# Performance work log

Measured on AMD Instinct MI355X. Metric: run time of the kernel, lower is better.

Reference implementation:

```python
import jax, jax.numpy as jnp
from jax import lax
import numpy as np

N3, N2, N1, N0 = 862, 1723, 3445, 6890  # mesh hierarchy (SMPL 6890 verts)
DEG, K = 16, 4  # nnz/row per Chebyshev support; K = order 3 + 1 supports


def _conv(x, w, b, s):
    y = lax.conv_general_dilated(x, w, (s, s), 'VALID', dimension_numbers=('NCHW', 'OIHW', 'NCHW'))
    return y + b[None, :, None, None]


def _pool(x):
    return lax.reduce_window(x, -jnp.inf, lax.max, (1, 1, 2, 2), (1, 1, 2, 2), 'VALID')


def _lin(x, w, b):
    return x @ w.T + b


def _rodrigues(r):  # [J,3] axis-angle -> [J,3,3] (batch_rodrigues)
    th = jnp.linalg.norm(r, axis=1, keepdims=True) + 1e-8
    k = r / th
    kx, ky, kz = k[:, 0], k[:, 1], k[:, 2]
    z = jnp.zeros_like(kx)
    Km = jnp.stack([z, -kz, ky, kz, z, -kx, -ky, kx, z], axis=1).reshape(-1, 3, 3)
    th = th[:, :, None]
    return jnp.eye(3, dtype=r.dtype)[None] + jnp.sin(th) * Km + (1.0 - jnp.cos(th)) * (Km @ Km)


def _spmm(idx, val, x):  # torch.sparse.mm with fixed nnz/row; idx,val: [N,D]
    return jnp.einsum('nd,ndf->nf', val, x[idx])


def _gcl(x, idx, val, W, b):  # Chebyshev graph conv: sum_k (A_k @ x) @ W_k + b
    return jnp.einsum('knd,kndf,kfo->no', val, x[idx], W) + b


def _basenet(frame, p):
    (c1w, c1b, c2w, c2b, c3w, c3b, c4w, c4b, c5w, c5b, fc1w, fc1b, fc4w, fc4b) = p
    c = _pool(jax.nn.relu(_conv(frame, c1w, c1b, 2)))
    c = _pool(jax.nn.relu(_conv(c, c2w, c2b, 1)))
    c = _pool(jax.nn.relu(_conv(c, c3w, c3b, 1)))
    c = _pool(jax.nn.relu(_conv(c, c4w, c4b, 1)))
    c = _pool(_conv(c, c5w, c5b, 1))  # [1,128,14,14]
    flat = jnp.transpose(c, (0, 3, 2, 1)).reshape(1, -1)  # torch.transpose(c,1,-1).reshape(1,-1)
    return _lin(flat, fc1w, fc1b), jax.nn.relu(_lin(flat, fc4w, fc4b))


def _forward(segmentations, poses, pose_mean, trans,
             c1w, c1b, c2w, c2b, c3w, c3b, c4w, c4b, c5w, c5b,
             fc1w, fc1b, fc2w, fc2b, fc3w, fc3b, fc4w, fc4b,
             fc5w, fc5b, fc6w, fc6b, fc7w, fc7b,
             gW3, gb3, gW2, gb2, gW1, gb1, gW0, gb0,
             av3, av2, av1, av0, uv2, uv1, uv0,
             ai3, ai2, ai1, ai0, ui2, ui1, ui0):
    nf = segmentations.shape[0]
    bp = (c1w, c1b, c2w, c2b, c3w, c3b, c4w, c4b, c5w, c5b, fc1w, fc1b, fc4w, fc4b)
    shape20, pose200 = jax.vmap(lambda f: _basenet(f, bp))(segmentations)  # [F,1,20],[F,1,200]
    pose_feat = jax.nn.relu(_lin(poses, fc5w, fc5b))  # [F,1,200]
    cat = jnp.concatenate([pose200, pose_feat], axis=-1)  # [F,1,400]
    pose_results = _lin(_lin(cat, fc6w, fc6b), fc7w, fc7b)  # [F,1,219]
    pm = pose_mean.at[:3].set(0.0)
    pose_init = _rodrigues(pm.reshape(-1, 3)).reshape(-1)  # [216]
    pct = jnp.concatenate([trans, pose_init])[None, None]  # [1,1,219]
    add = pose_results + pct
    add_poses = add[..., 3:].reshape(nf, -1, 24, 3, 3)
    add_trans = add[..., :3]
    betas_avr = shape20.reshape(-1, 20).mean(0)  # [20]
    betas_val = _lin(betas_avr, fc3w, fc3b)[None]  # [1,10]
    x = _lin(betas_avr, fc2w, fc2b).reshape(N3, 64)
    x = jax.nn.relu(_gcl(x, ai3, av3, gW3, gb3))  # [862,32]
    x = _spmm(ui2, uv2, x)                         # [1723,32]
    x = jax.nn.relu(_gcl(x, ai2, av2, gW2, gb2))  # [1723,16]
    x = _spmm(ui1, uv1, x)                         # [3445,16]
    x = jax.nn.relu(_gcl(x, ai1, av1, gW1, gb1))  # [3445,16]
    x = _spmm(ui0, uv0, x)                         # [6890,16]
    x = jnp.tanh(_gcl(x, ai0, av0, gW0, gb0))     # [6890,3]
    offsets = (x / 10.0)[None]
    return offsets, betas_val, add_poses, add_trans


def setup_inputs():
    ks = iter(jax.random.split(jax.random.key(0), 80))
    f32 = jnp.float32
    nrm = lambda shp, s: jax.random.normal(next(ks), shp, f32) * s
    uni = lambda shp, s: jax.random.uniform(next(ks), shp, f32) * s
    ri = lambda shp, hi: jax.random.randint(next(ks), shp, 0, hi)
    inp = {}
    inp['segmentations'] = nrm((8, 1, 3, 1017, 1017), 1.0)
    inp['poses'] = nrm((8, 1, 75), 1.0)
    inp['pose_mean'] = nrm((72,), 0.3)
    inp['trans'] = jnp.array([0.0, 0.2, -2.3], f32)
    for nm, shp, s in [('c1w', (8, 3, 3, 3), .1), ('c1b', (8,), .01), ('c2w', (16, 8, 3, 3), .1), ('c2b', (16,), .01),
                       ('c3w', (32, 16, 3, 3), .1), ('c3b', (32,), .01), ('c4w', (64, 32, 3, 3), .1), ('c4b', (64,), .01),
                       ('c5w', (128, 64, 3, 3), .1), ('c5b', (128,), .01),
                       ('fc1w', (20, 25088), .01), ('fc1b', (20,), .01), ('fc2w', (55168, 20), .05), ('fc2b', (55168,), .01),
                       ('fc3w', (10, 20), .05), ('fc3b', (10,), .01), ('fc4w', (200, 25088), .01), ('fc4b', (200,), .01),
                       ('fc5w', (200, 75), .05), ('fc5b', (200,), .01), ('fc6w', (100, 400), .05), ('fc6b', (100,), .01),
                       ('fc7w', (219, 100), .05), ('fc7b', (219,), .01),
                       ('gW3', (4, 64, 32), .1), ('gb3', (32,), .01), ('gW2', (4, 32, 16), .1), ('gb2', (16,), .01),
                       ('gW1', (4, 16, 16), .1), ('gb1', (16,), .01), ('gW0', (4, 16, 3), .1), ('gb0', (3,), .01)]:
        inp[nm] = nrm(shp, s)
    for nm, n in [('3', N3), ('2', N2), ('1', N1), ('0', N0)]:
        inp['av' + nm] = uni((K, n, DEG), 0.2)
        inp['ai' + nm] = ri((K, n, DEG), n)
    for nm, n_fine, n_coarse in [('2', N2, N3), ('1', N1, N2), ('0', N0, N1)]:
        inp['uv' + nm] = uni((n_fine, 4), 0.3)
        inp['ui' + nm] = ri((n_fine, 4), n_coarse)
    return inp


def reference(segmentations, poses, pose_mean, trans,
              c1w, c1b, c2w, c2b, c3w, c3b, c4w, c4b, c5w, c5b,
              fc1w, fc1b, fc2w, fc2b, fc3w, fc3b, fc4w, fc4b,
              fc5w, fc5b, fc6w, fc6b, fc7w, fc7b,
              gW3, gb3, gW2, gb2, gW1, gb1, gW0, gb0,
              av3, av2, av1, av0, uv2, uv1, uv0,
              ai3, ai2, ai1, ai0, ui2, ui1, ui0):
    return _forward(segmentations, poses, pose_mean, trans,
                    c1w, c1b, c2w, c2b, c3w, c3b, c4w, c4b, c5w, c5b,
                    fc1w, fc1b, fc2w, fc2b, fc3w, fc3b, fc4w, fc4b,
                    fc5w, fc5b, fc6w, fc6b, fc7w, fc7b,
                    gW3, gb3, gW2, gb2, gW1, gb1, gW0, gb0,
                    av3, av2, av1, av0, uv2, uv1, uv0,
                    ai3, ai2, ai1, ai0, ui2, ui1, ui0)
```

## Files before the change

### kernel.cpp

```cpp
#include <hip/hip_runtime.h>
#include <math.h>

__global__ __launch_bounds__(256) void conv1_lds(
    const float* __restrict__ in, const float* __restrict__ w,
    const float* __restrict__ bias, float* __restrict__ out)
{
    constexpr int Hin = 1017, P = 254;
    __shared__ float li[17][4][65];
    const int f  = blockIdx.y;
    const int ct = blockIdx.x & 3;
    const int rt = blockIdx.x >> 2;
    const int t  = threadIdx.x;
    const int lane = t & 63, wid = t >> 6;
    const int row0 = rt * 16, col0 = ct * 256;
    const float* inf = in + (size_t)f * 3 * Hin * Hin;

    const int ph = rt * 4 + wid, pw = ct * 64 + lane;
    const bool wactive = (ph < P) && (pw < P);

    float acc[32];
    #pragma unroll
    for (int i = 0; i < 32; i++) acc[i] = 0.f;

    for (int ic = 0; ic < 3; ic++) {
        __syncthreads();
        const float* src = inf + (size_t)ic * Hin * Hin;
        #pragma unroll
        for (int i = 0; i < 17; i++) {
            int gr = row0 + i; if (gr > Hin - 1) gr = Hin - 1;
            int gc = col0 + t; if (gc > Hin - 1) gc = Hin - 1;
            li[i][t & 3][t >> 2] = src[(size_t)gr * Hin + gc];
        }
        if (t < 17) {
            int gr = row0 + t; if (gr > Hin - 1) gr = Hin - 1;
            int gc = col0 + 256; if (gc > Hin - 1) gc = Hin - 1;
            li[t][0][64] = src[(size_t)gr * Hin + gc];
        }
        __syncthreads();

        float win[25];
        #pragma unroll
        for (int r = 0; r < 5; r++)
            #pragma unroll
            for (int c = 0; c < 5; c++)
                win[r * 5 + c] = li[4 * wid + r][c & 3][lane + (c >> 2)];

        #pragma unroll
        for (int oc = 0; oc < 8; oc++) {
            float wr[9];
            #pragma unroll
            for (int j = 0; j < 9; j++) wr[j] = w[(oc * 3 + ic) * 9 + j];
            #pragma unroll
            for (int py = 0; py < 2; py++)
                #pragma unroll
                for (int px = 0; px < 2; px++) {
                    float s = acc[(oc * 2 + py) * 2 + px];
                    #pragma unroll
                    for (int kh = 0; kh < 3; kh++)
                        #pragma unroll
                        for (int kw = 0; kw < 3; kw++)
                            s += wr[kh * 3 + kw] * win[(2 * py + kh) * 5 + (2 * px + kw)];
                    acc[(oc * 2 + py) * 2 + px] = s;
                }
        }
    }

    if (wactive) {
        #pragma unroll
        for (int oc = 0; oc < 8; oc++) {
            float m = fmaxf(fmaxf(acc[oc * 4 + 0], acc[oc * 4 + 1]),
                            fmaxf(acc[oc * 4 + 2], acc[oc * 4 + 3]));
            m = fmaxf(m + bias[oc], 0.f);
            out[(((size_t)f * 8 + oc) * P + ph) * P + pw] = m;
        }
    }
}

template<int IC, int OCG, bool RELU, bool FLATOUT>
__global__ __launch_bounds__(256) void conv_pool_s1(
    const float* __restrict__ in, const float* __restrict__ w,
    const float* __restrict__ bias, float* __restrict__ out,
    int Hin, int P, int OC)
{
    const int f = blockIdx.y, g = blockIdx.z;
    int tid = blockIdx.x * 256 + threadIdx.x;
    if (tid >= P * P) return;
    int ph = tid / P, pw = tid % P;
    const float* inf = in + ((size_t)f * IC) * Hin * Hin + (size_t)(2 * ph) * Hin + 2 * pw;
    const float* wg = w + (size_t)g * OCG * IC * 9;

    float acc[OCG * 4];
    #pragma unroll
    for (int i = 0; i < OCG * 4; i++) acc[i] = 0.f;

    for (int ic = 0; ic < IC; ic++) {
        const float* p = inf + (size_t)ic * Hin * Hin;
        float win[4][4];
        #pragma unroll
        for (int r = 0; r < 4; r++) {
            float2 a = *(const float2*)(p + (size_t)r * Hin);
            float2 b = *(const float2*)(p + (size_t)r * Hin + 2);
            win[r][0] = a.x; win[r][1] = a.y; win[r][2] = b.x; win[r][3] = b.y;
        }
        #pragma unroll
        for (int oc = 0; oc < OCG; oc++) {
            float wr[9];
            #pragma unroll
            for (int j = 0; j < 9; j++) wr[j] = wg[(oc * IC + ic) * 9 + j];
            #pragma unroll
            for (int py = 0; py < 2; py++)
                #pragma unroll
                for (int px = 0; px < 2; px++) {
                    float s = acc[(oc * 2 + py) * 2 + px];
                    #pragma unroll
                    for (int kh = 0; kh < 3; kh++)
                        #pragma unroll
                        for (int kw = 0; kw < 3; kw++)
                            s += wr[kh * 3 + kw] * win[py + kh][px + kw];
                    acc[(oc * 2 + py) * 2 + px] = s;
                }
        }
    }

    #pragma unroll
    for (int oc = 0; oc < OCG; oc++) {
        float m = fmaxf(fmaxf(acc[oc * 4 + 0], acc[oc * 4 + 1]),
                        fmaxf(acc[oc * 4 + 2], acc[oc * 4 + 3]));
        m += bias[g * OCG + oc];
        if (RELU) m = fmaxf(m, 0.f);
        int ocg = g * OCG + oc;
        if (FLATOUT) {
            out[(size_t)f * (P * P * OC) + (pw * P + ph) * OC + ocg] = m;
        } else {
            out[(((size_t)f * OC + ocg) * P + ph) * P + pw] = m;
        }
    }
}

__global__ __launch_bounds__(256) void fc_head(
    const float* __restrict__ flat,
    const float* __restrict__ fc1w, const float* __restrict__ fc1b,
    const float* __restrict__ fc4w, const float* __restrict__ fc4b,
    float* __restrict__ shape20, float* __restrict__ pose200)
{
    int o = blockIdx.x;
    const float* W = (o < 20) ? fc1w + (size_t)o * 25088
                              : fc4w + (size_t)(o - 20) * 25088;
    const float4* W4  = (const float4*)W;
    const float4* fl4 = (const float4*)flat;
    float acc[8];
    #pragma unroll
    for (int f = 0; f < 8; f++) acc[f] = 0.f;
    for (int i = threadIdx.x; i < 6272; i += 256) {
        float4 wv = W4[i];
        #pragma unroll
        for (int f = 0; f < 8; f++) {
            float4 xv = fl4[f * 6272 + i];
            acc[f] += wv.x * xv.x + wv.y * xv.y + wv.z * xv.z + wv.w * xv.w;
        }
    }
    #pragma unroll
    for (int f = 0; f < 8; f++)
        for (int off = 32; off > 0; off >>= 1)
            acc[f] += __shfl_down(acc[f], off, 64);
    __shared__ float red[4][8];
    int wid = threadIdx.x >> 6, lane = threadIdx.x & 63;
    if (lane == 0) {
        #pragma unroll
        for (int f = 0; f < 8; f++) red[wid][f] = acc[f];
    }
    __syncthreads();
    if (threadIdx.x < 8) {
        int f = threadIdx.x;
        float s = red[0][f] + red[1][f] + red[2][f] + red[3][f];
        if (o < 20) shape20[f * 20 + o] = s + fc1b[o];
        else        pose200[f * 200 + (o - 20)] = fmaxf(s + fc4b[o - 20], 0.f);
    }
}

__global__ __launch_bounds__(256) void pose_fc5(
    const float* __restrict__ poses,
    const float* __restrict__ fc5w, const float* __restrict__ fc5b,
    float* __restrict__ pose_feat)
{
    int t = blockIdx.x * 256 + threadIdx.x;
    if (t >= 8 * 200) return;
    int f = t / 200, o = t % 200;
    float s = fc5b[o];
    const float* pr = poses + f * 75;
    const float* wr = fc5w + o * 75;
    #pragma unroll 5
    for (int j = 0; j < 75; j++) s += pr[j] * wr[j];
    pose_feat[f * 200 + o] = fmaxf(s, 0.f);
}

__global__ __launch_bounds__(256) void pose_fc6(
    const float* __restrict__ pose200, const float* __restrict__ pose_feat,
    const float* __restrict__ fc6w, const float* __restrict__ fc6b,
    float* __restrict__ t1)
{
    int wv = blockIdx.x * 4 + (threadIdx.x >> 6);
    int lane = threadIdx.x & 63;
    if (wv >= 8 * 100) return;
    int f = wv / 100, o = wv % 100;
    float s = 0.f;
    for (int j = lane; j < 400; j += 64) {
        float xv = (j < 200) ? pose200[f * 200 + j] : pose_feat[f * 200 + (j - 200)];
        s += xv * fc6w[o * 400 + j];
    }
    #pragma unroll
    for (int off = 32; off > 0; off >>= 1) s += __shfl_down(s, off, 64);
    if (lane == 0) t1[f * 100 + o] = s + fc6b[o];
}

__global__ __launch_bounds__(256) void pose_fc7(
    const float* __restrict__ t1, const float* __restrict__ fc7w,
    const float* __restrict__ fc7b, const float* __restrict__ pose_mean,
    const float* __restrict__ trans, float* __restrict__ out)
{
    int wv = blockIdx.x * 4 + (threadIdx.x >> 6);
    int lane = threadIdx.x & 63;
    if (wv >= 8 * 219) return;
    int f = wv / 219, c = wv % 219;
    float s = 0.f;
    {
        float xv = t1[f * 100 + lane];
        s += xv * fc7w[c * 100 + lane];
        int j2 = lane + 64;
        if (j2 < 100) s += t1[f * 100 + j2] * fc7w[c * 100 + j2];
    }
    #pragma unroll
    for (int off = 32; off > 0; off >>= 1) s += __shfl_down(s, off, 64);
    if (lane != 0) return;
    s += fc7b[c];
    float pct;
    if (c < 3) {
        pct = trans[c];
    } else {
        int j = (c - 3) / 9, e = (c - 3) % 9;
        float rx = (j == 0) ? 0.f : pose_mean[3 * j + 0];
        float ry = (j == 0) ? 0.f : pose_mean[3 * j + 1];
        float rz = (j == 0) ? 0.f : pose_mean[3 * j + 2];
        float th = sqrtf(rx * rx + ry * ry + rz * rz) + 1e-8f;
        float kx = rx / th, ky = ry / th, kz = rz / th;
        float sn = sinf(th), c2 = 1.f - cosf(th);
        float R[9];
        R[0] = 1.f - c2 * (ky * ky + kz * kz);
        R[1] = -sn * kz + c2 * (kx * ky);
        R[2] =  sn * ky + c2 * (kx * kz);
        R[3] =  sn * kz + c2 * (kx * ky);
        R[4] = 1.f - c2 * (kx * kx + kz * kz);
        R[5] = -sn * kx + c2 * (ky * kz);
        R[6] = -sn * ky + c2 * (kx * kz);
        R[7] =  sn * kx + c2 * (ky * kz);
        R[8] = 1.f - c2 * (kx * kx + ky * ky);
        pct = R[e];
    }
    s += pct;
    if (c < 3) out[22408 + f * 3 + c] = s;
    else       out[20680 + f * 216 + (c - 3)] = s;
}

__global__ __launch_bounds__(256) void betas_fc2(
    const float* __restrict__ shape20,
    const float* __restrict__ fc2w, const float* __restrict__ fc2b,
    const float* __restrict__ fc3w, const float* __restrict__ fc3b,
    float* __restrict__ x0, float* __restrict__ out)
{
    __shared__ float avr[20];
    int t = threadIdx.x;
    if (t < 20) {
        float s = 0.f;
        for (int f = 0; f < 8; f++) s += shape20[f * 20 + t];
        avr[t] = s * 0.125f;
    }
    __syncthreads();
    int r = blockIdx.x * 256 + t;
    if (r < 55168) {
        float s = fc2b[r];
        #pragma unroll
        for (int j = 0; j < 20; j++) s += fc2w[(size_t)r * 20 + j] * avr[j];
        x0[r] = s;
    }
    if (blockIdx.x == 0 && t < 10) {
        float s = fc3b[t];
        for (int j = 0; j < 20; j++) s += fc3w[t * 20 + j] * avr[j];
        out[20670 + t] = s;
    }
}

template<int F, int O, int ACT>
__global__ __launch_bounds__(256) void gcl(
    const float* __restrict__ x, const int* __restrict__ ai,
    const float* __restrict__ av, const float* __restrict__ gW,
    const float* __restrict__ gb, float* __restrict__ y, int N)
{
    constexpr int VPW = 64 / F;
    constexpr int VPB = 4 * VPW;
    constexpr int HS  = 4 * F + 8;
    __shared__ float h[VPB][HS];

    int wid = threadIdx.x >> 6, lane = threadIdx.x & 63;
    {
        int vl = wid * VPW + (VPW == 1 ? 0 : lane / F);
        int fl = lane % F;
        int n = blockIdx.x * VPB + vl;
        if (n < N) {
            #pragma unroll
            for (int k = 0; k < 4; k++) {
                const int*   ip = ai + ((size_t)k * N + n) * 16;
                const float* vp = av + ((size_t)k * N + n) * 16;
                float s = 0.f;
                #pragma unroll
                for (int d = 0; d < 16; d++)
                    s += vp[d] * x[(size_t)ip[d] * F + fl];
                h[vl][k * F + fl] = s;
            }
        }
    }
    __syncthreads();

    int t = threadIdx.x;
    if (t < VPB * O) {
        int vl = t / O, o = t % O;
        int n = blockIdx.x * VPB + vl;
        if (n < N) {
            float s = gb[o];
            #pragma unroll
            for (int k = 0; k < 4; k++)
                for (int f2 = 0; f2 < F; f2++)
                    s += h[vl][k * F + f2] * gW[((size_t)k * F + f2) * O + o];
            if (ACT == 0) s = fmaxf(s, 0.f);
            else          s = tanhf(s) * 0.1f;
            y[(size_t)n * O + o] = s;
        }
    }
}

template<int F>
__global__ __launch_bounds__(256) void spmm(
    const float* __restrict__ x, const int* __restrict__ ui,
    const float* __restrict__ uv, float* __restrict__ y, int N)
{
    int t = blockIdx.x * 256 + threadIdx.x;
    if (t >= N * F) return;
    int n = t / F, f = t % F;
    float s = 0.f;
    #pragma unroll
    for (int j = 0; j < 4; j++)
        s += uv[n * 4 + j] * x[(size_t)ui[n * 4 + j] * F + f];
    y[t] = s;
}

extern "C" void kernel_launch(void* const* d_in, const int* in_sizes, int n_in,
                              void* d_out, int out_size, void* d_ws, size_t ws_size,
                              hipStream_t stream) {
    (void)in_sizes; (void)n_in; (void)out_size; (void)ws_size;

    const float* seg   = (const float*)d_in[0];
    const float* poses = (const float*)d_in[1];
    const float* pmean = (const float*)d_in[2];
    const float* trans = (const float*)d_in[3];
    const float* c1w = (const float*)d_in[4];  const float* c1b = (const float*)d_in[5];
    const float* c2w = (const float*)d_in[6];  const float* c2b = (const float*)d_in[7];
    const float* c3w = (const float*)d_in[8];  const float* c3b = (const float*)d_in[9];
    const float* c4w = (const float*)d_in[10]; const float* c4b = (const float*)d_in[11];
    const float* c5w = (const float*)d_in[12]; const float* c5b = (const float*)d_in[13];
    const float* fc1w = (const float*)d_in[14]; const float* fc1b = (const float*)d_in[15];
    const float* fc2w = (const float*)d_in[16]; const float* fc2b = (const float*)d_in[17];
    const float* fc3w = (const float*)d_in[18]; const float* fc3b = (const float*)d_in[19];
    const float* fc4w = (const float*)d_in[20]; const float* fc4b = (const float*)d_in[21];
    const float* fc5w = (const float*)d_in[22]; const float* fc5b = (const float*)d_in[23];
    const float* fc6w = (const float*)d_in[24]; const float* fc6b = (const float*)d_in[25];
    const float* fc7w = (const float*)d_in[26]; const float* fc7b = (const float*)d_in[27];
    const float* gW3 = (const float*)d_in[28]; const float* gb3 = (const float*)d_in[29];
    const float* gW2 = (const float*)d_in[30]; const float* gb2 = (const float*)d_in[31];
    const float* gW1 = (const float*)d_in[32]; const float* gb1 = (const float*)d_in[33];
    const float* gW0 = (const float*)d_in[34]; const float* gb0 = (const float*)d_in[35];
    const float* av3 = (const float*)d_in[36]; const int* ai3 = (const int*)d_in[37];
    const float* av2 = (const float*)d_in[38]; const int* ai2 = (const int*)d_in[39];
    const float* av1 = (const float*)d_in[40]; const int* ai1 = (const int*)d_in[41];
    const float* av0 = (const float*)d_in[42]; const int* ai0 = (const int*)d_in[43];
    const float* uv2 = (const float*)d_in[44]; const int* ui2 = (const int*)d_in[45];
    const float* uv1 = (const float*)d_in[46]; const int* ui1 = (const int*)d_in[47];
    const float* uv0 = (const float*)d_in[48]; const int* ui0 = (const int*)d_in[49];

    float* W = (float*)d_ws;
    float* out = (float*)d_out;

    float* pool1 = W + 0;
    float* pool2 = W + 4129024;
    float* pool3 = W + 0;
    float* pool4 = W + 4129024;
    float* flat5 = W + 4589824;
    float* shape20 = W + 1000000;
    float* pose200 = shape20 + 160;
    float* x0  = pose200 + 1600;
    float* y3  = x0 + 55168;
    float* x2  = y3 + 27584;
    float* y2  = x2 + 55136;
    float* x1  = y2 + 27568;
    float* y1  = x1 + 55120;
    float* x0u = y1 + 55120;
    float* pose_feat = x0u + 110240;
    float* t1 = pose_feat + 1600;

    conv1_lds<<<dim3(256, 8), 256, 0, stream>>>(seg, c1w, c1b, pool1);
    conv_pool_s1<8, 16, true, false>
        <<<dim3(63, 8, 1), 256, 0, stream>>>(pool1, c2w, c2b, pool2, 254, 126, 16);
    conv_pool_s1<16, 16, true, false>
        <<<dim3(16, 8, 2), 256, 0, stream>>>(pool2, c3w, c3b, pool3, 126, 62, 32);
    conv_pool_s1<32, 8, true, false>
        <<<dim3(4, 8, 8), 256, 0, stream>>>(pool3, c4w, c4b, pool4, 62, 30, 64);
    conv_pool_s1<64, 2, false, true>
        <<<dim3(1, 8, 64), 256, 0, stream>>>(pool4, c5w, c5b, flat5, 30, 14, 128);

    fc_head<<<dim3(220), 256, 0, stream>>>(flat5, fc1w, fc1b, fc4w, fc4b, shape20, pose200);
    pose_fc5<<<dim3(7),   256, 0, stream>>>(poses, fc5w, fc5b, pose_feat);
    pose_fc6<<<dim3(200), 256, 0, stream>>>(pose200, pose_feat, fc6w, fc6b, t1);
    pose_fc7<<<dim3(438), 256, 0, stream>>>(t1, fc7w, fc7b, pmean, trans, out);
    betas_fc2<<<dim3(216), 256, 0, stream>>>(shape20, fc2w, fc2b, fc3w, fc3b, x0, out);

    gcl<64, 32, 0><<<dim3(216),  256, 0, stream>>>(x0,  ai3, av3, gW3, gb3, y3, 862);
    spmm<32>      <<<dim3(216),  256, 0, stream>>>(y3,  ui2, uv2, x2, 1723);
    gcl<32, 16, 0><<<dim3(216),  256, 0, stream>>>(x2,  ai2, av2, gW2, gb2, y2, 1723);
    spmm<16>      <<<dim3(216),  256, 0, stream>>>(y2,  ui1, uv1, x1, 3445);
    gcl<16, 16, 0><<<dim3(216),  256, 0, stream>>>(x1,  ai1, av1, gW1, gb1, y1, 3445);
    spmm<16>      <<<dim3(431),  256, 0, stream>>>(y1,  ui0, uv0, x0u, 6890);
    gcl<16, 3, 1> <<<dim3(431),  256, 0, stream>>>(x0u, ai0, av0, gW0, gb0, out, 6890);
}
```

Measured before the change: 192.6 us.

## Merge small FC kernels into combined launches and halve conv output-channel groups

```diff
diff --git a/kernel.cpp b/kernel.cpp
--- a/kernel.cpp
+++ b/kernel.cpp
@@ -137,80 +137,111 @@
     }
 }
 
-__global__ __launch_bounds__(256) void fc_head(
+__global__ __launch_bounds__(256) void fc_head_plus(
     const float* __restrict__ flat,
     const float* __restrict__ fc1w, const float* __restrict__ fc1b,
     const float* __restrict__ fc4w, const float* __restrict__ fc4b,
-    float* __restrict__ shape20, float* __restrict__ pose200)
-{
-    int o = blockIdx.x;
-    const float* W = (o < 20) ? fc1w + (size_t)o * 25088
-                              : fc4w + (size_t)(o - 20) * 25088;
-    const float4* W4  = (const float4*)W;
-    const float4* fl4 = (const float4*)flat;
-    float acc[8];
-    #pragma unroll
-    for (int f = 0; f < 8; f++) acc[f] = 0.f;
-    for (int i = threadIdx.x; i < 6272; i += 256) {
-        float4 wv = W4[i];
-        #pragma unroll
-        for (int f = 0; f < 8; f++) {
-            float4 xv = fl4[f * 6272 + i];
-            acc[f] += wv.x * xv.x + wv.y * xv.y + wv.z * xv.z + wv.w * xv.w;
-        }
-    }
-    #pragma unroll
-    for (int f = 0; f < 8; f++)
-        for (int off = 32; off > 0; off >>= 1)
-            acc[f] += __shfl_down(acc[f], off, 64);
-    __shared__ float red[4][8];
-    int wid = threadIdx.x >> 6, lane = threadIdx.x & 63;
-    if (lane == 0) {
-        #pragma unroll
-        for (int f = 0; f < 8; f++) red[wid][f] = acc[f];
-    }
-    __syncthreads();
-    if (threadIdx.x < 8) {
-        int f = threadIdx.x;
-        float s = red[0][f] + red[1][f] + red[2][f] + red[3][f];
-        if (o < 20) shape20[f * 20 + o] = s + fc1b[o];
-        else        pose200[f * 200 + (o - 20)] = fmaxf(s + fc4b[o - 20], 0.f);
-    }
-}
-
-__global__ __launch_bounds__(256) void pose_fc5(
     const float* __restrict__ poses,
     const float* __restrict__ fc5w, const float* __restrict__ fc5b,
+    float* __restrict__ shape20, float* __restrict__ pose200,
     float* __restrict__ pose_feat)
 {
-    int t = blockIdx.x * 256 + threadIdx.x;
-    if (t >= 8 * 200) return;
-    int f = t / 200, o = t % 200;
-    float s = fc5b[o];
-    const float* pr = poses + f * 75;
-    const float* wr = fc5w + o * 75;
-    #pragma unroll 5
-    for (int j = 0; j < 75; j++) s += pr[j] * wr[j];
-    pose_feat[f * 200 + o] = fmaxf(s, 0.f);
-}
-
-__global__ __launch_bounds__(256) void pose_fc6(
+    int o = blockIdx.x;
+    if (o < 220) {
+        const float* W = (o < 20) ? fc1w + (size_t)o * 25088
+                                  : fc4w + (size_t)(o - 20) * 25088;
+        const float4* W4  = (const float4*)W;
+        const float4* fl4 = (const float4*)flat;
+        float acc[8];
+        #pragma unroll
+        for (int f = 0; f < 8; f++) acc[f] = 0.f;
+        for (int i = threadIdx.x; i < 6272; i += 256) {
+            float4 wv = W4[i];
+            #pragma unroll
+            for (int f = 0; f < 8; f++) {
+                float4 xv = fl4[f * 6272 + i];
+                acc[f] += wv.x * xv.x + wv.y * xv.y + wv.z * xv.z + wv.w * xv.w;
+            }
+        }
+        #pragma unroll
+        for (int f = 0; f < 8; f++)
+            for (int off = 32; off > 0; off >>= 1)
+                acc[f] += __shfl_down(acc[f], off, 64);
+        __shared__ float red[4][8];
+        int wid = threadIdx.x >> 6, lane = threadIdx.x & 63;
+        if (lane == 0) {
+            #pragma unroll
+            for (int f = 0; f < 8; f++) red[wid][f] = acc[f];
+        }
+        __syncthreads();
+        if (threadIdx.x < 8) {
+            int f = threadIdx.x;
+            float s = red[0][f] + red[1][f] + red[2][f] + red[3][f];
+            if (o < 20) shape20[f * 20 + o] = s + fc1b[o];
+            else        pose200[f * 200 + (o - 20)] = fmaxf(s + fc4b[o - 20], 0.f);
+        }
+    } else {
+        int t = (o - 220) * 256 + threadIdx.x;
+        if (t >= 8 * 200) return;
+        int f = t / 200, oo = t % 200;
+        float s = fc5b[oo];
+        const float* pr = poses + f * 75;
+        const float* wr = fc5w + oo * 75;
+        #pragma unroll 5
+        for (int j = 0; j < 75; j++) s += pr[j] * wr[j];
+        pose_feat[f * 200 + oo] = fmaxf(s, 0.f);
+    }
+}
+
+__global__ __launch_bounds__(256) void mid_fused(
+    const float* __restrict__ shape20,
+    const float* __restrict__ fc2w, const float* __restrict__ fc2b,
+    const float* __restrict__ fc3w, const float* __restrict__ fc3b,
+    float* __restrict__ x0, float* __restrict__ out,
     const float* __restrict__ pose200, const float* __restrict__ pose_feat,
     const float* __restrict__ fc6w, const float* __restrict__ fc6b,
     float* __restrict__ t1)
 {
-    int wv = blockIdx.x * 4 + (threadIdx.x >> 6);
-    int lane = threadIdx.x & 63;
-    if (wv >= 8 * 100) return;
-    int f = wv / 100, o = wv % 100;
-    float s = 0.f;
-    for (int j = lane; j < 400; j += 64) {
-        float xv = (j < 200) ? pose200[f * 200 + j] : pose_feat[f * 200 + (j - 200)];
-        s += xv * fc6w[o * 400 + j];
-    }
-    #pragma unroll
-    for (int off = 32; off > 0; off >>= 1) s += __shfl_down(s, off, 64);
-    if (lane == 0) t1[f * 100 + o] = s + fc6b[o];
+    int b = blockIdx.x, t = threadIdx.x;
+    if (b < 216) {
+        __shared__ float avr[20];
+        if (t < 20) {
+            float s = 0.f;
+            for (int f = 0; f < 8; f++) s += shape20[f * 20 + t];
+            avr[t] = s * 0.125f;
+        }
+        __syncthreads();
+        int r = b * 256 + t;
+        if (r < 55168) {
+            float s = fc2b[r];
+            const float4* w4 = (const float4*)(fc2w + (size_t)r * 20);
+            #pragma unroll
+            for (int q = 0; q < 5; q++) {
+                float4 wv = w4[q];
+                s += wv.x * avr[q * 4 + 0] + wv.y * avr[q * 4 + 1]
+                   + wv.z * avr[q * 4 + 2] + wv.w * avr[q * 4 + 3];
+            }
+            x0[r] = s;
+        }
+        if (b == 0 && t < 10) {
+            float s = fc3b[t];
+            for (int j = 0; j < 20; j++) s += fc3w[t * 20 + j] * avr[j];
+            out[20670 + t] = s;
+        }
+    } else {
+        int wv = (b - 216) * 4 + (t >> 6);
+        int lane = t & 63;
+        if (wv >= 8 * 100) return;
+        int f = wv / 100, o = wv % 100;
+        float s = 0.f;
+        for (int j = lane; j < 400; j += 64) {
+            float xv = (j < 200) ? pose200[f * 200 + j] : pose_feat[f * 200 + (j - 200)];
+            s += xv * fc6w[o * 400 + j];
+        }
+        #pragma unroll
+        for (int off = 32; off > 0; off >>= 1) s += __shfl_down(s, off, 64);
+        if (lane == 0) t1[f * 100 + o] = s + fc6b[o];
+    }
 }
 
 __global__ __launch_bounds__(256) void pose_fc7(
@@ -259,34 +290,6 @@
     s += pct;
     if (c < 3) out[22408 + f * 3 + c] = s;
     else       out[20680 + f * 216 + (c - 3)] = s;
-}
-
-__global__ __launch_bounds__(256) void betas_fc2(
-    const float* __restrict__ shape20,
-    const float* __restrict__ fc2w, const float* __restrict__ fc2b,
-    const float* __restrict__ fc3w, const float* __restrict__ fc3b,
-    float* __restrict__ x0, float* __restrict__ out)
-{
-    __shared__ float avr[20];
-    int t = threadIdx.x;
-    if (t < 20) {
-        float s = 0.f;
-        for (int f = 0; f < 8; f++) s += shape20[f * 20 + t];
-        avr[t] = s * 0.125f;
-    }
-    __syncthreads();
-    int r = blockIdx.x * 256 + t;
-    if (r < 55168) {
-        float s = fc2b[r];
-        #pragma unroll
-        for (int j = 0; j < 20; j++) s += fc2w[(size_t)r * 20 + j] * avr[j];
-        x0[r] = s;
-    }
-    if (blockIdx.x == 0 && t < 10) {
-        float s = fc3b[t];
-        for (int j = 0; j < 20; j++) s += fc3w[t * 20 + j] * avr[j];
-        out[20670 + t] = s;
-    }
 }
 
 template<int F, int O, int ACT>
@@ -406,20 +409,21 @@
     float* t1 = pose_feat + 1600;
 
     conv1_lds<<<dim3(256, 8), 256, 0, stream>>>(seg, c1w, c1b, pool1);
-    conv_pool_s1<8, 16, true, false>
-        <<<dim3(63, 8, 1), 256, 0, stream>>>(pool1, c2w, c2b, pool2, 254, 126, 16);
-    conv_pool_s1<16, 16, true, false>
-        <<<dim3(16, 8, 2), 256, 0, stream>>>(pool2, c3w, c3b, pool3, 126, 62, 32);
-    conv_pool_s1<32, 8, true, false>
-        <<<dim3(4, 8, 8), 256, 0, stream>>>(pool3, c4w, c4b, pool4, 62, 30, 64);
+    conv_pool_s1<8, 8, true, false>
+        <<<dim3(63, 8, 2), 256, 0, stream>>>(pool1, c2w, c2b, pool2, 254, 126, 16);
+    conv_pool_s1<16, 8, true, false>
+        <<<dim3(16, 8, 4), 256, 0, stream>>>(pool2, c3w, c3b, pool3, 126, 62, 32);
+    conv_pool_s1<32, 4, true, false>
+        <<<dim3(4, 8, 16), 256, 0, stream>>>(pool3, c4w, c4b, pool4, 62, 30, 64);
     conv_pool_s1<64, 2, false, true>
         <<<dim3(1, 8, 64), 256, 0, stream>>>(pool4, c5w, c5b, flat5, 30, 14, 128);
 
-    fc_head<<<dim3(220), 256, 0, stream>>>(flat5, fc1w, fc1b, fc4w, fc4b, shape20, pose200);
-    pose_fc5<<<dim3(7),   256, 0, stream>>>(poses, fc5w, fc5b, pose_feat);
-    pose_fc6<<<dim3(200), 256, 0, stream>>>(pose200, pose_feat, fc6w, fc6b, t1);
+    fc_head_plus<<<dim3(227), 256, 0, stream>>>(flat5, fc1w, fc1b, fc4w, fc4b,
+                                                poses, fc5w, fc5b,
+                                                shape20, pose200, pose_feat);
+    mid_fused<<<dim3(416), 256, 0, stream>>>(shape20, fc2w, fc2b, fc3w, fc3b, x0, out,
+                                             pose200, pose_feat, fc6w, fc6b, t1);
     pose_fc7<<<dim3(438), 256, 0, stream>>>(t1, fc7w, fc7b, pmean, trans, out);
-    betas_fc2<<<dim3(216), 256, 0, stream>>>(shape20, fc2w, fc2b, fc3w, fc3b, x0, out);
 
     gcl<64, 32, 0><<<dim3(216),  256, 0, stream>>>(x0,  ai3, av3, gW3, gb3, y3, 862);
     spmm<32>      <<<dim3(216),  256, 0, stream>>>(y3,  ui2, uv2, x2, 1723);
```

New measurement: 170.0 us. 11.7% less time.
